# Performance work log

Measured on AMD Instinct MI355X. Metric: run time of the kernel, lower is better.

The kernel has to match this reference:

```python
import jax, jax.numpy as jnp
import numpy as np

B, E, I, H = 131072, 13, 13, 64  # batch, features(output_size), input_size, hidden_size
G = 4 * H  # i,f,g,o gates stacked (torch LSTM order)


def setup_inputs() -> dict:
    key = jax.random.key(0)
    k = jax.random.split(key, 7)
    s = 1.0 / np.sqrt(H)  # torch default uniform bound scale
    return {
        "x": jax.random.normal(k[0], (B, E, I), dtype=jnp.float32),
        "W_ih": jax.random.uniform(k[1], (E, G, I), jnp.float32, -s, s),
        "W_hh": jax.random.uniform(k[2], (E, G, H), jnp.float32, -s, s),  # multiplies h0=0
        "b_ih": jax.random.uniform(k[3], (E, G), jnp.float32, -s, s),
        "b_hh": jax.random.uniform(k[4], (E, G), jnp.float32, -s, s),
        "W_lin": jax.random.uniform(k[5], (E, H), jnp.float32, -s, s),
        "b_lin": jax.random.uniform(k[6], (E,), jnp.float32, -s, s),
    }


def reference(x, W_ih, W_hh, b_ih, b_hh, W_lin, b_lin):
    # seq_len == 1 and h0 = c0 = 0, so W_hh @ h0 = 0 and c = f*c0 + i*g = i*g.
    gates = jnp.einsum("bei,ehi->beh", x, W_ih) + b_ih + b_hh  # [B, E, 4H]
    i_g, f_g, g_g, o_g = jnp.split(gates, 4, axis=-1)  # torch gate order i,f,g,o
    c = jax.nn.sigmoid(i_g) * jnp.tanh(g_g)  # [B, E, H]
    h = jax.nn.sigmoid(o_g) * jnp.tanh(c)  # [B, E, H]
    out = jax.nn.sigmoid(jnp.einsum("beh,eh->be", h, W_lin) + b_lin)  # [B, E]
    return out
```

## Files before the change

kernel.cpp:

```cpp
#include <hip/hip_runtime.h>


#define E_N 13
#define I_N 13
#define H_N 64
#define G_N 256
#define ROWS_PER_BLOCK 512

typedef _Float16 half8 __attribute__((ext_vector_type(8)));
typedef float f32x16 __attribute__((ext_vector_type(16)));

__device__ __forceinline__ float fast_rcp(float x) { return __builtin_amdgcn_rcpf(x); }
__device__ __forceinline__ float fast_exp(float x) { return __expf(x); }
__device__ __forceinline__ float sigmoid_f(float x) { return fast_rcp(1.0f + fast_exp(-x)); }
__device__ __forceinline__ float tanh_f(float x) { return 1.0f - 2.0f * fast_rcp(fast_exp(2.0f * x) + 1.0f); }

__global__ __launch_bounds__(256, 4) void music_lstm_mfma(
    const float* __restrict__ x,
    const float* __restrict__ W_ih,
    const float* __restrict__ b_ih,
    const float* __restrict__ b_hh,
    const float* __restrict__ W_lin,
    const float* __restrict__ b_lin,
    float* __restrict__ out,
    int n_b)
{
    const int e     = blockIdx.x;
    const int tileb = blockIdx.y;
    const int tid   = threadIdx.x;
    const int lane  = tid & 63;
    const int wave  = tid >> 6;
    const int lrow  = lane & 31;
    const int khalf = lane >> 5;
    const int koff  = khalf * 8;

    __shared__ float lds_wl[H_N];
    if (tid < H_N) lds_wl[tid] = W_lin[e * H_N + tid];
    __syncthreads();

    const float blin_e = b_lin[e];

    half8 wf[6];
#pragma unroll
    for (int g = 0; g < 3; ++g) {
        const int gbase = (g == 0) ? 0 : (g == 1) ? 2 * H_N : 3 * H_N;
#pragma unroll
        for (int hb = 0; hb < 2; ++hb) {
            const int row = gbase + hb * 32 + lrow;
            const float* wr = W_ih + ((size_t)e * G_N + row) * I_N;
            const float bias = b_ih[e * G_N + row] + b_hh[e * G_N + row];
            half8 f;
#pragma unroll
            for (int j = 0; j < 8; ++j) {
                const int k = koff + j;
                const float v = (k < I_N) ? wr[k] : ((k == I_N) ? bias : 0.0f);
                f[j] = (_Float16)v;
            }
            wf[hb * 3 + g] = f;
        }
    }

    const int b_wave = tileb * ROWS_PER_BLOCK + wave * 128;

    for (int it = 0; it < 4; ++it) {
        const int b0 = b_wave + it * 32;
        const int bb = (b0 + lrow < n_b) ? (b0 + lrow) : (n_b - 1);

        const float* xb = x + (size_t)bb * (E_N * I_N) + e * I_N;
        half8 xf;
#pragma unroll
        for (int j = 0; j < 8; ++j) {
            const int k = koff + j;
            const float v = (k < I_N) ? xb[k] : ((k == I_N) ? 1.0f : 0.0f);
            xf[j] = (_Float16)v;
        }

        float partial = 0.0f;
#pragma unroll
        for (int hb = 0; hb < 2; ++hb) {
            f32x16 zz;
#pragma unroll
            for (int q = 0; q < 16; ++q) zz[q] = 0.0f;
            const f32x16 ai = __builtin_amdgcn_mfma_f32_32x32x16_f16(wf[hb * 3 + 0], xf, zz, 0, 0, 0);
            const f32x16 ag = __builtin_amdgcn_mfma_f32_32x32x16_f16(wf[hb * 3 + 1], xf, zz, 0, 0, 0);
            const f32x16 ao = __builtin_amdgcn_mfma_f32_32x32x16_f16(wf[hb * 3 + 2], xf, zz, 0, 0, 0);
#pragma unroll
            for (int r = 0; r < 16; ++r) {
                const int h = hb * 32 + (r & 3) + 8 * (r >> 2) + 4 * khalf;
                const float c  = sigmoid_f(ai[r]) * tanh_f(ag[r]);
                const float hh = sigmoid_f(ao[r]) * tanh_f(c);
                partial = fmaf(hh, lds_wl[h], partial);
            }
        }

        const float pre = partial + __shfl_xor(partial, 32) + blin_e;
        if (lane < 32 && b0 + lrow < n_b)
            out[(size_t)(b0 + lrow) * E_N + e] = sigmoid_f(pre);
    }
}

extern "C" void kernel_launch(void* const* d_in, const int* in_sizes, int n_in,
                              void* d_out, int out_size, void* d_ws, size_t ws_size,
                              hipStream_t stream) {
    const float* x     = (const float*)d_in[0];
    const float* W_ih  = (const float*)d_in[1];
    const float* b_ih  = (const float*)d_in[3];
    const float* b_hh  = (const float*)d_in[4];
    const float* W_lin = (const float*)d_in[5];
    const float* b_lin = (const float*)d_in[6];
    float* out = (float*)d_out;

    const int n_b = in_sizes[0] / (E_N * I_N);
    dim3 grid(E_N, (n_b + ROWS_PER_BLOCK - 1) / ROWS_PER_BLOCK);

    music_lstm_mfma<<<grid, 256, 0, stream>>>(x, W_ih, b_ih, b_hh, W_lin, b_lin, out, n_b);
}
```

Before: 233.7 us.

## Prefetch next x tile, merge sigmoid-tanh reciprocals, and swap grid axes

Loads the next 32-row x slice into registers while the current slice goes through the MFMA and activations, to hide global load latency. Each sigmoid*tanh product now uses a single reciprocal of the product of the two denominators, cutting the number of rcp instructions. The grid is transposed so the batch tile is the fast axis, which changes which blocks run together and their locality on x. The fused formula can overflow for large gate values where exp goes to infinity (inf*inf gives NaN), which is a numerical risk.

```diff
diff --git a/kernel.cpp b/kernel.cpp
--- a/kernel.cpp
+++ b/kernel.cpp
@@ -12,8 +12,6 @@
 
 __device__ __forceinline__ float fast_rcp(float x) { return __builtin_amdgcn_rcpf(x); }
 __device__ __forceinline__ float fast_exp(float x) { return __expf(x); }
-__device__ __forceinline__ float sigmoid_f(float x) { return fast_rcp(1.0f + fast_exp(-x)); }
-__device__ __forceinline__ float tanh_f(float x) { return 1.0f - 2.0f * fast_rcp(fast_exp(2.0f * x) + 1.0f); }
 
 __global__ __launch_bounds__(256, 4) void music_lstm_mfma(
     const float* __restrict__ x,
@@ -25,8 +23,8 @@
     float* __restrict__ out,
     int n_b)
 {
-    const int e     = blockIdx.x;
-    const int tileb = blockIdx.y;
+    const int tileb = blockIdx.x;
+    const int e     = blockIdx.y;
     const int tid   = threadIdx.x;
     const int lane  = tid & 63;
     const int wave  = tid >> 6;
@@ -62,18 +60,35 @@
 
     const int b_wave = tileb * ROWS_PER_BLOCK + wave * 128;
 
-    for (int it = 0; it < 4; ++it) {
-        const int b0 = b_wave + it * 32;
-        const int bb = (b0 + lrow < n_b) ? (b0 + lrow) : (n_b - 1);
-
+    float xn[8];
+    {
+        const int br = b_wave + lrow;
+        const int bb = (br < n_b) ? br : (n_b - 1);
         const float* xb = x + (size_t)bb * (E_N * I_N) + e * I_N;
-        half8 xf;
 #pragma unroll
         for (int j = 0; j < 8; ++j) {
             const int k = koff + j;
-            const float v = (k < I_N) ? xb[k] : ((k == I_N) ? 1.0f : 0.0f);
-            xf[j] = (_Float16)v;
+            xn[j] = (k < I_N) ? xb[k] : ((k == I_N) ? 1.0f : 0.0f);
         }
+    }
+
+#pragma unroll
+    for (int it = 0; it < 4; ++it) {
+        float xnext[8];
+        if (it < 3) {
+            const int br = b_wave + (it + 1) * 32 + lrow;
+            const int bb = (br < n_b) ? br : (n_b - 1);
+            const float* xb = x + (size_t)bb * (E_N * I_N) + e * I_N;
+#pragma unroll
+            for (int j = 0; j < 8; ++j) {
+                const int k = koff + j;
+                xnext[j] = (k < I_N) ? xb[k] : ((k == I_N) ? 1.0f : 0.0f);
+            }
+        }
+
+        half8 xh;
+#pragma unroll
+        for (int j = 0; j < 8; ++j) xh[j] = (_Float16)xn[j];
 
         float partial = 0.0f;
 #pragma unroll
@@ -81,21 +96,29 @@
             f32x16 zz;
 #pragma unroll
             for (int q = 0; q < 16; ++q) zz[q] = 0.0f;
-            const f32x16 ai = __builtin_amdgcn_mfma_f32_32x32x16_f16(wf[hb * 3 + 0], xf, zz, 0, 0, 0);
-            const f32x16 ag = __builtin_amdgcn_mfma_f32_32x32x16_f16(wf[hb * 3 + 1], xf, zz, 0, 0, 0);
-            const f32x16 ao = __builtin_amdgcn_mfma_f32_32x32x16_f16(wf[hb * 3 + 2], xf, zz, 0, 0, 0);
+            const f32x16 ai = __builtin_amdgcn_mfma_f32_32x32x16_f16(wf[hb * 3 + 0], xh, zz, 0, 0, 0);
+            const f32x16 ag = __builtin_amdgcn_mfma_f32_32x32x16_f16(wf[hb * 3 + 1], xh, zz, 0, 0, 0);
+            const f32x16 ao = __builtin_amdgcn_mfma_f32_32x32x16_f16(wf[hb * 3 + 2], xh, zz, 0, 0, 0);
 #pragma unroll
             for (int r = 0; r < 16; ++r) {
                 const int h = hb * 32 + (r & 3) + 8 * (r >> 2) + 4 * khalf;
-                const float c  = sigmoid_f(ai[r]) * tanh_f(ag[r]);
-                const float hh = sigmoid_f(ao[r]) * tanh_f(c);
+                const float ei = fast_exp(-ai[r]);
+                const float eg = fast_exp(2.0f * ag[r]);
+                const float c  = (eg - 1.0f) * fast_rcp((1.0f + ei) * (1.0f + eg));
+                const float eo = fast_exp(-ao[r]);
+                const float ec = fast_exp(2.0f * c);
+                const float hh = (ec - 1.0f) * fast_rcp((1.0f + eo) * (1.0f + ec));
                 partial = fmaf(hh, lds_wl[h], partial);
             }
         }
 
         const float pre = partial + __shfl_xor(partial, 32) + blin_e;
-        if (lane < 32 && b0 + lrow < n_b)
-            out[(size_t)(b0 + lrow) * E_N + e] = sigmoid_f(pre);
+        const int bo = b_wave + it * 32 + lrow;
+        if (lane < 32 && bo < n_b)
+            out[(size_t)bo * E_N + e] = fast_rcp(1.0f + fast_exp(-pre));
+
+#pragma unroll
+        for (int j = 0; j < 8; ++j) xn[j] = xnext[j];
     }
 }
 
@@ -111,7 +134,7 @@
     float* out = (float*)d_out;
 
     const int n_b = in_sizes[0] / (E_N * I_N);
-    dim3 grid(E_N, (n_b + ROWS_PER_BLOCK - 1) / ROWS_PER_BLOCK);
+    dim3 grid((n_b + ROWS_PER_BLOCK - 1) / ROWS_PER_BLOCK, E_N);
 
     music_lstm_mfma<<<grid, 256, 0, stream>>>(x, W_ih, b_ih, b_hh, W_lin, b_lin, out, n_b);
 }
```

New measurement: 226.4 us. 1.03x faster.
